# Optimization experiments

Measured on AMD Instinct MI355X. Metric: run time of the kernel, lower is better.

## Reference

```python
import jax, jax.numpy as jnp
import numpy as np

B, C, H, W = 8, 64, 256, 256  # H must equal W (matmul shape constraint in original)


def setup_inputs() -> dict:
    key = jax.random.key(0)
    ks = jax.random.split(key, 7)
    s = 1.0 / np.sqrt(C)  # fan-in scaled init, like conv default scale
    return {
        "x": jax.random.normal(ks[0], (B, C, H, W), dtype=jnp.float32),
        "Wq": jax.random.normal(ks[1], (C, C), dtype=jnp.float32) * s,
        "bq": jax.random.normal(ks[2], (C,), dtype=jnp.float32) * s,
        "Wk": jax.random.normal(ks[3], (C, C), dtype=jnp.float32) * s,
        "bk": jax.random.normal(ks[4], (C,), dtype=jnp.float32) * s,
        "Wv": jax.random.normal(ks[5], (C, C), dtype=jnp.float32) * s,
        "bv": jax.random.normal(ks[6], (C,), dtype=jnp.float32) * s,
    }


def _conv1x1(x, Wt, b):
    # 1x1 Conv2d == per-pixel GEMM over channels: [o,c] x [b,c,h,w] -> [b,o,h,w]
    return jnp.einsum("oc,bchw->bohw", Wt, x) + b[None, :, None, None]


def reference(x, Wq, bq, Wk, bk, Wv, bv):
    q = _conv1x1(x, Wq, bq)
    k = _conv1x1(x, Wk, bk)
    v = _conv1x1(x, Wv, bv)
    # attn[b,c,i,j] = sum_h q[b,c,h,i] * k[b,c,h,j]   (q^T @ k over spatial)
    attn = jnp.einsum("bchi,bchj->bcij", q, k)
    # softmax over the CHANNEL axis (dim=-3 in torch == axis 1 here)
    attn = jax.nn.softmax(attn, axis=1)
    # out[b,c,i,j] = sum_m attn[b,c,i,m] * v[b,c,m,j]  (requires H == W)
    out = jnp.einsum("bcim,bcmj->bcij", attn, v)
    return out
```

## Files before the change

kernel.cpp:

```cpp
#include <hip/hip_runtime.h>
#include <math.h>

constexpr int CH  = 64;
constexpr int WW  = 256;
constexpr int HWS = WW * WW;
constexpr int NB  = 8;

typedef __attribute__((ext_vector_type(8))) short bf16x8;
typedef __attribute__((ext_vector_type(4))) float f32x4;

__device__ inline ushort f2bf(float f) {
    uint u = __float_as_uint(f);
    u += 0x7fffu + ((u >> 16) & 1u);
    return (ushort)(u >> 16);
}

__global__ __launch_bounds__(256) void qkv_kernel2(
    const float* __restrict__ x,
    const float* __restrict__ Wq, const float* __restrict__ bq,
    const float* __restrict__ Wk, const float* __restrict__ bk,
    const float* __restrict__ Wv, const float* __restrict__ bv,
    float* __restrict__ Q, float* __restrict__ K, ushort* __restrict__ V)
{
    __shared__ float Wt[64][192];
    __shared__ float Bias[192];
    __shared__ float Xs[8][128];

    const int tid = threadIdx.x;
    const int n0  = blockIdx.x * 128;
    const int b   = n0 >> 16;
    const int pb  = n0 & 65535;

    {
        const float* Wsrc[3] = {Wq, Wk, Wv};
#pragma unroll
        for (int mat = 0; mat < 3; ++mat) {
#pragma unroll
            for (int r = 0; r < 4; ++r) {
                const int flat = r * 256 + tid;
                const int o    = flat & 63;
                const int c4   = (flat >> 6) * 4;
                const float4 w = *(const float4*)&Wsrc[mat][o * 64 + c4];
                Wt[c4 + 0][mat * 64 + o] = w.x;
                Wt[c4 + 1][mat * 64 + o] = w.y;
                Wt[c4 + 2][mat * 64 + o] = w.z;
                Wt[c4 + 3][mat * 64 + o] = w.w;
            }
        }
        if (tid < 192)
            Bias[tid] = (tid < 64) ? bq[tid] : ((tid < 128) ? bk[tid - 64] : bv[tid - 128]);
    }

    const int mg  = tid >> 5;
    const int ng  = tid & 31;
    const int m0  = mg * 24;
    const int pix = ng * 4;

    float4 acc[24];
#pragma unroll
    for (int m = 0; m < 24; ++m) acc[m] = make_float4(0.f, 0.f, 0.f, 0.f);

    const int skk = tid >> 5;
    const int sp4 = (tid & 31) * 4;

    for (int c0 = 0; c0 < CH; c0 += 8) {
        __syncthreads();
        *(float4*)&Xs[skk][sp4] =
            *(const float4*)&x[((size_t)(b * CH + c0 + skk) << 16) + pb + sp4];
        __syncthreads();

#pragma unroll
        for (int kk = 0; kk < 8; ++kk) {
            float wv[24];
#pragma unroll
            for (int q4 = 0; q4 < 6; ++q4)
                *(float4*)&wv[q4 * 4] = *(const float4*)&Wt[c0 + kk][m0 + q4 * 4];
            const float4 xv = *(const float4*)&Xs[kk][pix];
#pragma unroll
            for (int m = 0; m < 24; ++m) {
                acc[m].x = fmaf(wv[m], xv.x, acc[m].x);
                acc[m].y = fmaf(wv[m], xv.y, acc[m].y);
                acc[m].z = fmaf(wv[m], xv.z, acc[m].z);
                acc[m].w = fmaf(wv[m], xv.w, acc[m].w);
            }
        }
    }

#pragma unroll
    for (int m = 0; m < 24; ++m) {
        const int gm  = m0 + m;
        const int mat = gm >> 6;
        const int ch  = gm & 63;
        const float bias = Bias[gm];
        float4 r = acc[m];
        r.x += bias; r.y += bias; r.z += bias; r.w += bias;
        const size_t oidx = ((size_t)(b * CH + ch) << 16) + pb + pix;
        if (mat == 0)      *(float4*)&Q[oidx] = r;
        else if (mat == 1) *(float4*)&K[oidx] = r;
        else {
            ushort4 vs;
            vs.x = f2bf(r.x); vs.y = f2bf(r.y); vs.z = f2bf(r.z); vs.w = f2bf(r.w);
            *(ushort4*)&V[oidx] = vs;
        }
    }
}

union FragU { uint u[4]; bf16x8 v; };

__device__ inline void frag_split(const float* __restrict__ S, int col, int quad,
                                  bf16x8* hi, bf16x8* lo) {
    FragU H, L;
#pragma unroll
    for (int rp = 0; rp < 4; ++rp) {
        const int h0 = quad * 8 + rp * 2;
        const int sw = ((h0 >> 1) & 7) << 2;
        const int c  = col ^ sw;
        const float f0 = S[(h0    ) * 128 + c];
        const float f1 = S[(h0 + 1) * 128 + c];
        const uint u0 = __float_as_uint(f0);
        const uint u1 = __float_as_uint(f1);
        const float g0 = f0 - __uint_as_float(u0 & 0xffff0000u);
        const float g1 = f1 - __uint_as_float(u1 & 0xffff0000u);
        H.u[rp] = __builtin_amdgcn_perm(u1, u0, 0x07060302u);
        L.u[rp] = __builtin_amdgcn_perm(__float_as_uint(g1), __float_as_uint(g0),
                                        0x07060302u);
    }
    *hi = H.v; *lo = L.v;
}

__global__ __launch_bounds__(256, 3) void attn_mfma(
    const float* __restrict__ Q, const float* __restrict__ Kt,
    float* __restrict__ attn)
{
    const int gid = blockIdx.x;
    const int bc  = gid >> 2;
    const int i0  = ((gid >> 1) & 1) * 128;
    const int j0  = (gid & 1) * 128;
    const float* q = Q  + (size_t)bc * HWS;
    const float* k = Kt + (size_t)bc * HWS;
    float* out     = attn + (size_t)bc * HWS;

    __shared__ float As[32 * 128];
    __shared__ float Bs[32 * 128];

    const int tid  = threadIdx.x;
    const int L    = tid & 63;
    const int wid  = tid >> 6;
    const int wy   = (wid >> 1) * 64;
    const int wx   = (wid & 1) * 64;
    const int ml   = L & 15;
    const int quad = L >> 4;

    f32x4 zero = {0.f, 0.f, 0.f, 0.f};
    f32x4 acc[4][4];
#pragma unroll
    for (int a = 0; a < 4; ++a)
#pragma unroll
        for (int b = 0; b < 4; ++b) acc[a][b] = zero;

    for (int k0 = 0; k0 < WW; k0 += 32) {
#pragma unroll
        for (int p = 0; p < 4; ++p) {
            const int flat = p * 256 + tid;
            const int hh   = flat >> 5;
            const int i4   = (flat & 31) * 4;
            const int sw   = ((hh >> 1) & 7) << 2;
            *(float4*)&As[hh * 128 + (i4 ^ sw)] =
                *(const float4*)&q[(size_t)(k0 + hh) * WW + i0 + i4];
            *(float4*)&Bs[hh * 128 + (i4 ^ sw)] =
                *(const float4*)&k[(size_t)(k0 + hh) * WW + j0 + i4];
        }
        __syncthreads();

        bf16x8 bh[4], bl[4];
#pragma unroll
        for (int t = 0; t < 4; ++t)
            frag_split(Bs, wx + t * 16 + ml, quad, &bh[t], &bl[t]);
#pragma unroll
        for (int a = 0; a < 4; ++a) {
            bf16x8 ah, al;
            frag_split(As, wy + a * 16 + ml, quad, &ah, &al);
#pragma unroll
            for (int b = 0; b < 4; ++b) {
                acc[a][b] = __builtin_amdgcn_mfma_f32_16x16x32_bf16(ah, bh[b], acc[a][b], 0, 0, 0);
                acc[a][b] = __builtin_amdgcn_mfma_f32_16x16x32_bf16(ah, bl[b], acc[a][b], 0, 0, 0);
                acc[a][b] = __builtin_amdgcn_mfma_f32_16x16x32_bf16(al, bh[b], acc[a][b], 0, 0, 0);
            }
        }
        __syncthreads();
    }

#pragma unroll
    for (int a = 0; a < 4; ++a)
#pragma unroll
        for (int b = 0; b < 4; ++b)
#pragma unroll
            for (int r = 0; r < 4; ++r)
                out[(size_t)(i0 + wy + a * 16 + quad * 4 + r) * WW
                    + j0 + wx + b * 16 + ml] = acc[a][b][r];
}

__global__ __launch_bounds__(256) void transpose_v(
    const ushort* __restrict__ Vb, ushort* __restrict__ Vt)
{
    const int blk = blockIdx.x;
    const int bc  = blk >> 2;
    const int m0  = ((blk >> 1) & 1) * 128;
    const int j0  = (blk & 1) * 128;
    const ushort* src = Vb + (size_t)bc * HWS;
    ushort* dst       = Vt + (size_t)bc * HWS;

    __shared__ ushort T[128][128] __attribute__((aligned(16)));

    const int tid = threadIdx.x;
#pragma unroll
    for (int p = 0; p < 8; ++p) {
        const int id  = p * 256 + tid;
        const int mm  = id >> 4;
        const int c16 = id & 15;
        const int cg  = (c16 + (mm >> 3)) & 15;
        *(uint4*)&T[mm][cg * 8] =
            *(const uint4*)(src + (size_t)(m0 + mm) * WW + j0 + c16 * 8);
    }
    __syncthreads();
#pragma unroll
    for (int p = 0; p < 4; ++p) {
        const int id  = p * 256 + tid;
        const int c16 = id & 15;
        const int jjp = id >> 4;
        const int jj  = jjp * 2;
        const int jjg = jj >> 3;
        ushort ra[8], rb[8];
#pragma unroll
        for (int u = 0; u < 8; ++u) {
            const int mm = c16 * 8 + u;
            const int cg = (jjg + c16) & 15;
            const uint pr = *(const uint*)&T[mm][cg * 8 + (jj & 7)];
            ra[u] = (ushort)(pr & 0xffffu);
            rb[u] = (ushort)(pr >> 16);
        }
        *(uint4*)(dst + (size_t)(j0 + jj)     * WW + m0 + c16 * 8) = *(uint4*)ra;
        *(uint4*)(dst + (size_t)(j0 + jj + 1) * WW + m0 + c16 * 8) = *(uint4*)rb;
    }
}

__global__ __launch_bounds__(128) void softmax_kernel(
    const float* __restrict__ logits, ushort* __restrict__ Wb)
{
    const int gid = blockIdx.x;
    const int b   = gid >> 8;
    const int i   = gid & 255;
    const int j2  = threadIdx.x * 2;
    const size_t off = (((size_t)(b * CH)) << 16) + (size_t)i * WW + j2;
    const float* base = logits + off;
    ushort* wout      = Wb + off;

    float2 v[CH];
#pragma unroll
    for (int c = 0; c < CH; ++c) v[c] = *(const float2*)&base[((size_t)c) << 16];

    float mx = v[0].x, my = v[0].y;
#pragma unroll
    for (int c = 1; c < CH; ++c) { mx = fmaxf(mx, v[c].x); my = fmaxf(my, v[c].y); }

    float sx = 0.f, sy = 0.f;
#pragma unroll
    for (int c = 0; c < CH; ++c) {
        v[c].x = __expf(v[c].x - mx); sx += v[c].x;
        v[c].y = __expf(v[c].y - my); sy += v[c].y;
    }
    const float ix = 1.0f / sx, iy = 1.0f / sy;
#pragma unroll
    for (int c = 0; c < CH; ++c) {
        ushort2 o;
        o.x = f2bf(v[c].x * ix);
        o.y = f2bf(v[c].y * iy);
        *(ushort2*)&wout[((size_t)c) << 16] = o;
    }
}

__global__ __launch_bounds__(256) void pv_kernel2(
    const ushort* __restrict__ Wb, const ushort* __restrict__ Vt,
    float* __restrict__ out)
{
    const int blk = blockIdx.x;
    const int bc  = blk >> 2;
    const int i0  = ((blk >> 1) & 1) * 128;
    const int j0  = (blk & 1) * 128;
    const ushort* w  = Wb + (size_t)bc * HWS;
    const ushort* vt = Vt + (size_t)bc * HWS;
    float* o         = out + (size_t)bc * HWS;

    __shared__ ushort As[128][40] __attribute__((aligned(16)));
    __shared__ ushort Bs[128][40] __attribute__((aligned(16)));

    const int tid  = threadIdx.x;
    const int L    = tid & 63;
    const int wid  = tid >> 6;
    const int wy   = (wid >> 1) * 64;
    const int wx   = (wid & 1) * 64;
    const int ml   = L & 15;
    const int quad = L >> 4;

    f32x4 zero = {0.f, 0.f, 0.f, 0.f};
    f32x4 acc[4][4];
#pragma unroll
    for (int a = 0; a < 4; ++a)
#pragma unroll
        for (int b = 0; b < 4; ++b) acc[a][b] = zero;

    for (int m0 = 0; m0 < WW; m0 += 32) {
#pragma unroll
        for (int p = 0; p < 2; ++p) {
            const int id  = p * 256 + tid;
            const int row = id >> 2;
            const int c4  = id & 3;
            *(uint4*)&As[row][c4 * 8] =
                *(const uint4*)(w  + (size_t)(i0 + row) * WW + m0 + c4 * 8);
            *(uint4*)&Bs[row][c4 * 8] =
                *(const uint4*)(vt + (size_t)(j0 + row) * WW + m0 + c4 * 8);
        }
        __syncthreads();

        bf16x8 af[4], bfr[4];
#pragma unroll
        for (int t = 0; t < 4; ++t)
            af[t]  = *(const bf16x8*)&As[wy + t * 16 + ml][quad * 8];
#pragma unroll
        for (int t = 0; t < 4; ++t)
            bfr[t] = *(const bf16x8*)&Bs[wx + t * 16 + ml][quad * 8];
#pragma unroll
        for (int a = 0; a < 4; ++a)
#pragma unroll
            for (int b = 0; b < 4; ++b)
                acc[a][b] = __builtin_amdgcn_mfma_f32_16x16x32_bf16(
                    af[a], bfr[b], acc[a][b], 0, 0, 0);
        __syncthreads();
    }

#pragma unroll
    for (int a = 0; a < 4; ++a)
#pragma unroll
        for (int b = 0; b < 4; ++b)
#pragma unroll
            for (int r = 0; r < 4; ++r)
                o[(size_t)(i0 + wy + a * 16 + quad * 4 + r) * WW
                  + j0 + wx + b * 16 + ml] = acc[a][b][r];
}

extern "C" void kernel_launch(void* const* d_in, const int* in_sizes, int n_in,
                              void* d_out, int out_size, void* d_ws, size_t ws_size,
                              hipStream_t stream) {
    const float* x  = (const float*)d_in[0];
    const float* Wq = (const float*)d_in[1];
    const float* bq = (const float*)d_in[2];
    const float* Wk = (const float*)d_in[3];
    const float* bk = (const float*)d_in[4];
    const float* Wv = (const float*)d_in[5];
    const float* bv = (const float*)d_in[6];
    float* out = (float*)d_out;

    const size_t NEL = (size_t)NB * CH * HWS;
    float*  Q  = (float*)d_ws;
    float*  K  = Q + NEL;
    ushort* Vb = (ushort*)(K + NEL);
    ushort* Vt = Vb + NEL;
    ushort* Wb = (ushort*)d_ws;

    qkv_kernel2<<<(NB * HWS) / 128, 256, 0, stream>>>(x, Wq, bq, Wk, bk, Wv, bv, Q, K, Vb);
    attn_mfma<<<NB * CH * 4, 256, 0, stream>>>(Q, K, out);
    transpose_v<<<NB * CH * 4, 256, 0, stream>>>(Vb, Vt);
    softmax_kernel<<<NB * WW, 128, 0, stream>>>(out, Wb);
    pv_kernel2<<<NB * CH * 4, 256, 0, stream>>>(Wb, Vt, out);
}
```

Measured before the change: 701.8 us.

## Compute QKV projection with split-bf16 MFMA instead of scalar FP32 FMA

Replaces the FP32 FMA-based 1x1 conv QKV kernel with an MFMA version. Weights and inputs are split into bf16 hi/lo pairs and combined with three MFMAs to keep near-FP32 accuracy. Weights are loaded straight into register fragments, and x is staged into swizzled LDS as hi/lo bf16. This targets the ALU cost of the projection, at the price of 16-lane-strided scalar output stores that may coalesce less well than the old float4 stores.

```diff
diff --git a/kernel.cpp b/kernel.cpp
--- a/kernel.cpp
+++ b/kernel.cpp
@@ -15,97 +15,135 @@
     return (ushort)(u >> 16);
 }
 
-__global__ __launch_bounds__(256) void qkv_kernel2(
+union FragU { uint u[4]; bf16x8 v; };
+
+__global__ __launch_bounds__(256) void qkv_mfma(
     const float* __restrict__ x,
     const float* __restrict__ Wq, const float* __restrict__ bq,
     const float* __restrict__ Wk, const float* __restrict__ bk,
     const float* __restrict__ Wv, const float* __restrict__ bv,
     float* __restrict__ Q, float* __restrict__ K, ushort* __restrict__ V)
 {
-    __shared__ float Wt[64][192];
-    __shared__ float Bias[192];
-    __shared__ float Xs[8][128];
-
-    const int tid = threadIdx.x;
-    const int n0  = blockIdx.x * 128;
-    const int b   = n0 >> 16;
-    const int pb  = n0 & 65535;
-
-    {
-        const float* Wsrc[3] = {Wq, Wk, Wv};
-#pragma unroll
-        for (int mat = 0; mat < 3; ++mat) {
-#pragma unroll
-            for (int r = 0; r < 4; ++r) {
-                const int flat = r * 256 + tid;
-                const int o    = flat & 63;
-                const int c4   = (flat >> 6) * 4;
-                const float4 w = *(const float4*)&Wsrc[mat][o * 64 + c4];
-                Wt[c4 + 0][mat * 64 + o] = w.x;
-                Wt[c4 + 1][mat * 64 + o] = w.y;
-                Wt[c4 + 2][mat * 64 + o] = w.z;
-                Wt[c4 + 3][mat * 64 + o] = w.w;
+    __shared__ ushort Xhi[128 * 64] __attribute__((aligned(16)));
+    __shared__ ushort Xlo[128 * 64] __attribute__((aligned(16)));
+
+    const int tid  = threadIdx.x;
+    const int ln   = tid & 63;
+    const int wid  = tid >> 6;
+    const int ml   = ln & 15;
+    const int quad = ln >> 4;
+
+    const int n0 = blockIdx.x * 128;
+    const int b  = n0 >> 16;
+    const int pb = n0 & 65535;
+    const float* xb = x + ((size_t)(b * CH) << 16);
+
+    bf16x8 Ah[3][2], Al[3][2];
+    float biasv[3][4];
+#pragma unroll
+    for (int a = 0; a < 3; ++a) {
+        const int mt = wid * 3 + a;
+        const float* Wsrc = (mt < 4) ? Wq : (mt < 8) ? Wk : Wv;
+        const float* bsrc = (mt < 4) ? bq : (mt < 8) ? bk : bv;
+        const int o = (mt & 3) * 16 + ml;
+#pragma unroll
+        for (int kf = 0; kf < 2; ++kf) {
+            FragU Hh, Ll;
+#pragma unroll
+            for (int rp = 0; rp < 4; ++rp) {
+                const float f0 = Wsrc[o * 64 + kf * 32 + quad * 8 + rp * 2];
+                const float f1 = Wsrc[o * 64 + kf * 32 + quad * 8 + rp * 2 + 1];
+                const uint u0 = __float_as_uint(f0);
+                const uint u1 = __float_as_uint(f1);
+                const float g0 = f0 - __uint_as_float(u0 & 0xffff0000u);
+                const float g1 = f1 - __uint_as_float(u1 & 0xffff0000u);
+                Hh.u[rp] = __builtin_amdgcn_perm(u1, u0, 0x07060302u);
+                Ll.u[rp] = __builtin_amdgcn_perm(__float_as_uint(g1),
+                                                 __float_as_uint(g0), 0x07060302u);
             }
-        }
-        if (tid < 192)
-            Bias[tid] = (tid < 64) ? bq[tid] : ((tid < 128) ? bk[tid - 64] : bv[tid - 128]);
-    }
-
-    const int mg  = tid >> 5;
-    const int ng  = tid & 31;
-    const int m0  = mg * 24;
-    const int pix = ng * 4;
-
-    float4 acc[24];
-#pragma unroll
-    for (int m = 0; m < 24; ++m) acc[m] = make_float4(0.f, 0.f, 0.f, 0.f);
-
-    const int skk = tid >> 5;
-    const int sp4 = (tid & 31) * 4;
-
-    for (int c0 = 0; c0 < CH; c0 += 8) {
-        __syncthreads();
-        *(float4*)&Xs[skk][sp4] =
-            *(const float4*)&x[((size_t)(b * CH + c0 + skk) << 16) + pb + sp4];
-        __syncthreads();
-
-#pragma unroll
-        for (int kk = 0; kk < 8; ++kk) {
-            float wv[24];
-#pragma unroll
-            for (int q4 = 0; q4 < 6; ++q4)
-                *(float4*)&wv[q4 * 4] = *(const float4*)&Wt[c0 + kk][m0 + q4 * 4];
-            const float4 xv = *(const float4*)&Xs[kk][pix];
-#pragma unroll
-            for (int m = 0; m < 24; ++m) {
-                acc[m].x = fmaf(wv[m], xv.x, acc[m].x);
-                acc[m].y = fmaf(wv[m], xv.y, acc[m].y);
-                acc[m].z = fmaf(wv[m], xv.z, acc[m].z);
-                acc[m].w = fmaf(wv[m], xv.w, acc[m].w);
+            Ah[a][kf] = Hh.v; Al[a][kf] = Ll.v;
+        }
+#pragma unroll
+        for (int r = 0; r < 4; ++r)
+            biasv[a][r] = bsrc[(mt & 3) * 16 + quad * 4 + r];
+    }
+
+#pragma unroll
+    for (int p = 0; p < 8; ++p) {
+        const int flat = p * 256 + tid;
+        const int c    = flat >> 5;
+        const int px4  = (flat & 31) * 4;
+        const float4 xv = *(const float4*)&xb[((size_t)c << 16) + pb + px4];
+#pragma unroll
+        for (int u = 0; u < 4; ++u) {
+            const int px = px4 + u;
+            const float f = (&xv.x)[u];
+            const uint fu = __float_as_uint(f);
+            const float lo = f - __uint_as_float(fu & 0xffff0000u);
+            const int adr = px * 64 + ((((c >> 3) ^ ((px >> 1) & 7))) << 3) + (c & 7);
+            Xhi[adr] = (ushort)(fu >> 16);
+            Xlo[adr] = (ushort)(__float_as_uint(lo) >> 16);
+        }
+    }
+    __syncthreads();
+
+    f32x4 acc[3][8];
+    const f32x4 zero = {0.f, 0.f, 0.f, 0.f};
+#pragma unroll
+    for (int a = 0; a < 3; ++a)
+#pragma unroll
+        for (int t = 0; t < 8; ++t) acc[a][t] = zero;
+
+#pragma unroll
+    for (int t = 0; t < 8; ++t) {
+        const int px = t * 16 + ml;
+        bf16x8 Bh[2], Bl[2];
+#pragma unroll
+        for (int kf = 0; kf < 2; ++kf) {
+            const int g   = kf * 4 + quad;
+            const int adr = px * 64 + ((g ^ ((px >> 1) & 7)) << 3);
+            Bh[kf] = *(const bf16x8*)&Xhi[adr];
+            Bl[kf] = *(const bf16x8*)&Xlo[adr];
+        }
+#pragma unroll
+        for (int a = 0; a < 3; ++a) {
+#pragma unroll
+            for (int kf = 0; kf < 2; ++kf) {
+                acc[a][t] = __builtin_amdgcn_mfma_f32_16x16x32_bf16(Ah[a][kf], Bh[kf], acc[a][t], 0, 0, 0);
+                acc[a][t] = __builtin_amdgcn_mfma_f32_16x16x32_bf16(Ah[a][kf], Bl[kf], acc[a][t], 0, 0, 0);
+                acc[a][t] = __builtin_amdgcn_mfma_f32_16x16x32_bf16(Al[a][kf], Bh[kf], acc[a][t], 0, 0, 0);
             }
         }
     }
 
 #pragma unroll
-    for (int m = 0; m < 24; ++m) {
-        const int gm  = m0 + m;
-        const int mat = gm >> 6;
-        const int ch  = gm & 63;
-        const float bias = Bias[gm];
-        float4 r = acc[m];
-        r.x += bias; r.y += bias; r.z += bias; r.w += bias;
-        const size_t oidx = ((size_t)(b * CH + ch) << 16) + pb + pix;
-        if (mat == 0)      *(float4*)&Q[oidx] = r;
-        else if (mat == 1) *(float4*)&K[oidx] = r;
-        else {
-            ushort4 vs;
-            vs.x = f2bf(r.x); vs.y = f2bf(r.y); vs.z = f2bf(r.z); vs.w = f2bf(r.w);
-            *(ushort4*)&V[oidx] = vs;
-        }
-    }
-}
-
-union FragU { uint u[4]; bf16x8 v; };
+    for (int a = 0; a < 3; ++a) {
+        const int mt = wid * 3 + a;
+        const int ch = (mt & 3) * 16 + quad * 4;
+        if (mt < 4) {
+#pragma unroll
+            for (int t = 0; t < 8; ++t)
+#pragma unroll
+                for (int r = 0; r < 4; ++r)
+                    Q[((size_t)(b * CH + ch + r) << 16) + pb + t * 16 + ml] =
+                        acc[a][t][r] + biasv[a][r];
+        } else if (mt < 8) {
+#pragma unroll
+            for (int t = 0; t < 8; ++t)
+#pragma unroll
+                for (int r = 0; r < 4; ++r)
+                    K[((size_t)(b * CH + ch + r) << 16) + pb + t * 16 + ml] =
+                        acc[a][t][r] + biasv[a][r];
+        } else {
+#pragma unroll
+            for (int t = 0; t < 8; ++t)
+#pragma unroll
+                for (int r = 0; r < 4; ++r)
+                    V[((size_t)(b * CH + ch + r) << 16) + pb + t * 16 + ml] =
+                        f2bf(acc[a][t][r] + biasv[a][r]);
+        }
+    }
+}
 
 __device__ inline void frag_split(const float* __restrict__ S, int col, int quad,
                                   bf16x8* hi, bf16x8* lo) {
@@ -367,7 +405,7 @@
     ushort* Vt = Vb + NEL;
     ushort* Wb = (ushort*)d_ws;
 
-    qkv_kernel2<<<(NB * HWS) / 128, 256, 0, stream>>>(x, Wq, bq, Wk, bk, Wv, bv, Q, K, Vb);
+    qkv_mfma<<<(NB * HWS) / 128, 256, 0, stream>>>(x, Wq, bq, Wk, bk, Wv, bv, Q, K, Vb);
     attn_mfma<<<NB * CH * 4, 256, 0, stream>>>(Q, K, out);
     transpose_v<<<NB * CH * 4, 256, 0, stream>>>(Vb, Vt);
     softmax_kernel<<<NB * WW, 128, 0, stream>>>(out, Wb);
```

After: 615.3 us. -12.3%, faster.
